# Kernel tuning notes

Measured on AMD Instinct MI355X. Metric: run time of the kernel, lower is better.

Reference implementation:

```python
import jax, jax.numpy as jnp
import numpy as np

DIM = 1024
H = 8            # heads (light and heavy)
DH = 64          # dim_head
W = 64           # local attention window (light_window_size // 2)
NQ = 512         # num_heavy_tokens_q
NKV = 1024       # num_heavy_tokens_kv
EPS = 1.0        # coor descent eps
NITERS = 50      # coor descent iters
FETCH = 9.0 / 8.0
SCALE = DH ** -0.5


def _ln(x, w, b):
    m = x.mean(-1, keepdims=True)
    v = ((x - m) ** 2).mean(-1, keepdims=True)
    return (x - m) * jax.lax.rsqrt(v + 1e-5) * w + b


def _rms(x, g):
    n = jnp.maximum(jnp.linalg.norm(x, axis=-1, keepdims=True), 1e-12)
    return x / n * np.sqrt(DIM).astype(np.float32) * g


def local_attn(x, Wqkv, Wout):
    # LocalMHA, non-causal, look_backward=1, look_forward=1, window W
    b, n, _ = x.shape
    nw = n // W
    qkv = x @ Wqkv.T                      # [b,n,3*H*DH]
    q, k, v = jnp.split(qkv, 3, axis=-1)
    def towin(t):
        return t.reshape(b, nw, W, H, DH).transpose(0, 3, 1, 2, 4)  # [b,h,nw,w,dh]
    q, k, v = map(towin, (q, k, v))
    def expand(t):  # gather prev/cur/next windows -> [b,h,nw,3w,dh]
        tp = jnp.pad(t, ((0, 0), (0, 0), (1, 1), (0, 0), (0, 0)))
        return jnp.concatenate([tp[:, :, :-2], tp[:, :, 1:-1], tp[:, :, 2:]], axis=3)
    ke, ve = expand(k), expand(v)
    sim = jnp.einsum('bhnid,bhnjd->bhnij', q, ke) * SCALE
    win = jnp.arange(nw)
    valid = jnp.concatenate([
        jnp.repeat((win > 0)[:, None], W, 1),
        jnp.ones((nw, W), bool),
        jnp.repeat((win < nw - 1)[:, None], W, 1)], axis=1)  # [nw,3w]
    sim = jnp.where(valid[None, None, :, None, :], sim, -1e9)
    attn = jax.nn.softmax(sim, axis=-1)
    o = jnp.einsum('bhnij,bhnjd->bhnid', attn, ve)
    o = o.transpose(0, 2, 3, 1, 4).reshape(b, n, H * DH)
    return o @ Wout.T


def route(x, routing_token, num_tokens):
    # CoordinateDescentRouter with num_routing_tokens=1, straight_through=True
    s = jnp.einsum('bnd,rd->brn', x, routing_token).reshape(x.shape[0], x.shape[1])
    n = s.shape[-1]
    logk = jnp.log(jnp.asarray(min(num_tokens * FETCH, float(n)), s.dtype))
    def body(ab, _):
        a, bb = ab
        a = EPS * (logk - jax.nn.logsumexp((s + bb) / EPS, axis=-1, keepdims=True))
        bb = -jax.nn.relu(s + a)
        return (a, bb), None
    (a, bb), _ = jax.lax.scan(body, (jnp.zeros((s.shape[0], 1), s.dtype), -s), None, length=NITERS)
    scores = jnp.exp((s + a + bb) / EPS)
    sel_scores, sel_idx = jax.lax.top_k(scores, num_tokens)
    # straight-through: forward value 1.0, gradient of identity
    sel_scores = sel_scores + jax.lax.stop_gradient(1.0 - sel_scores)
    return sel_scores, sel_idx


def heavy_attn(xq, ctx, scores_kv, gamma, Wq, Wkv, Wout, null_kv):
    b = xq.shape[0]
    xq = _rms(xq, gamma)
    ctx = _rms(ctx, gamma)
    q = (xq @ Wq.T).reshape(b, -1, H, DH).transpose(0, 2, 1, 3)           # [b,h,nq,dh]
    kv = (ctx @ Wkv.T).reshape(b, -1, H, 2 * DH).transpose(0, 2, 1, 3)    # [b,h,nkv,2dh]
    k, v = kv[..., :DH], kv[..., DH:]
    v = v * scores_kv[:, None, :, None]
    nk = jnp.broadcast_to(null_kv[0][None, :, None, :], (b, H, 1, DH))
    nv = jnp.broadcast_to(null_kv[1][None, :, None, :], (b, H, 1, DH))
    k = jnp.concatenate([nk, k], axis=2)
    v = jnp.concatenate([nv, v], axis=2)
    sim = jnp.einsum('bhid,bhjd->bhij', q, k) * SCALE
    attn = jax.nn.softmax(sim, axis=-1)
    o = jnp.einsum('bhij,bhjd->bhid', attn, v)
    o = o.transpose(0, 2, 1, 3).reshape(b, -1, H * DH)
    return o @ Wout.T


def setup_inputs() -> dict:
    key = jax.random.key(0)
    ks = jax.random.split(key, 12)
    D, IN = DIM, H * DH
    w = lambda k, shape: jax.random.normal(k, shape, jnp.float32) * 0.02
    return {
        'x': jax.random.normal(ks[0], (4, 4096, D), jnp.float32),
        'ln_w': jnp.ones((D,), jnp.float32),
        'ln_b': jnp.zeros((D,), jnp.float32),
        'Wqkv': w(ks[1], (3 * IN, D)),
        'Wout_l': w(ks[2], (D, IN)),
        'rt_q': jax.random.normal(ks[3], (1, D), jnp.float32),
        'rt_kv': jax.random.normal(ks[4], (1, D), jnp.float32),
        'gamma': jnp.ones((D,), jnp.float32),
        'Wq': w(ks[5], (IN, D)),
        'Wkv': w(ks[6], (2 * IN, D)),
        'Wout_h': w(ks[7], (D, IN)),
        'null_kv': jax.random.normal(ks[8], (2, H, DH), jnp.float32),
        'null_q': jax.random.normal(ks[9], (D,), jnp.float32),
    }


def reference(x, ln_w, ln_b, Wqkv, Wout_l, rt_q, rt_kv, gamma, Wq, Wkv, Wout_h, null_kv, null_q):
    b, n, d = x.shape
    light = local_attn(_ln(x, ln_w, ln_b), Wqkv, Wout_l)
    sq, iq = route(x, rt_q, NQ)
    skv, ikv = route(x, rt_kv, NKV)
    br = jnp.arange(b)[:, None]
    xq = x[br, iq]          # gather routed queries  [b,NQ,d]
    xkv = x[br, ikv]        # gather routed kv       [b,NKV,d]
    heavy = heavy_attn(xq, xkv, skv, gamma, Wq, Wkv, Wout_h, null_kv)
    heavy = heavy * sq[..., None]
    out = jnp.broadcast_to(null_q[None, None, :], (b, n, d))
    out = out.at[br, iq].set(heavy)   # scatter heavy branch back
    return out + light
```

## Files before the change

kernel.cpp:

```cpp
#include <hip/hip_runtime.h>
#include <hip/hip_bf16.h>

typedef __attribute__((ext_vector_type(8))) short bv8;
typedef __attribute__((ext_vector_type(4))) float fv4;
typedef __hip_bfloat16 bf16;

#define MFMA16(a,b,c) __builtin_amdgcn_mfma_f32_16x16x32_bf16((a),(b),(c),0,0,0)
#define GLOAD_LDS(gp, lp) __builtin_amdgcn_global_load_lds( \
    (const __attribute__((address_space(1))) void*)(gp), \
    (__attribute__((address_space(3))) void*)(lp), 16, 0, 0)

template<int NW>
__device__ __forceinline__ float blockReduceSumF(float v) {
  #pragma unroll
  for (int m = 1; m < 64; m <<= 1) v += __shfl_xor(v, m, 64);
  __shared__ float sm[NW];
  if ((threadIdx.x & 63) == 0) sm[threadIdx.x >> 6] = v;
  __syncthreads();
  float t = 0.f;
  #pragma unroll
  for (int i = 0; i < NW; ++i) t += sm[i];
  __syncthreads();
  return t;
}

template<int NW>
__device__ __forceinline__ double blockReduceMaxD(double v) {
  #pragma unroll
  for (int m = 1; m < 64; m <<= 1) v = fmax(v, __shfl_xor(v, m, 64));
  __shared__ double sm[NW];
  if ((threadIdx.x & 63) == 0) sm[threadIdx.x >> 6] = v;
  __syncthreads();
  double t = sm[0];
  #pragma unroll
  for (int i = 1; i < NW; ++i) t = fmax(t, sm[i]);
  __syncthreads();
  return t;
}

__global__ __launch_bounds__(256)
void prep_kernel(const float* __restrict__ x, const float* __restrict__ lnw,
                 const float* __restrict__ lnb, const float* __restrict__ rtq,
                 const float* __restrict__ rtkv, bf16* __restrict__ lnout,
                 double* __restrict__ s,
                 const float* __restrict__ a0, const float* __restrict__ a1,
                 const float* __restrict__ a2, const float* __restrict__ a3,
                 const float* __restrict__ a4,
                 bf16* __restrict__ b0, bf16* __restrict__ b1, bf16* __restrict__ b2,
                 bf16* __restrict__ b3, bf16* __restrict__ b4,
                 int* __restrict__ posq) {
  const int bid = blockIdx.x;
  if (bid < 16384) {
    const int r = bid;
    const float* xr = x + (size_t)r * 1024;
    float v4[4]; float ssum = 0.f;
    double dq = 0.0, dk = 0.0;
    #pragma unroll
    for (int i = 0; i < 4; ++i) {
      int d = threadIdx.x + i * 256;
      float v = xr[d];
      v4[i] = v; ssum += v;
      dq += (double)v * (double)rtq[d];
      dk += (double)v * (double)rtkv[d];
    }
    ssum = blockReduceSumF<4>(ssum);
    const float mean = ssum * (1.0f / 1024.0f);
    float vs = 0.f;
    #pragma unroll
    for (int i = 0; i < 4; ++i) { float d = v4[i] - mean; vs += d * d; }
    vs = blockReduceSumF<4>(vs);
    const float rstd = 1.0f / sqrtf(vs * (1.0f / 1024.0f) + 1e-5f);
    #pragma unroll
    for (int m = 1; m < 64; m <<= 1) { dq += __shfl_xor(dq, m, 64); dk += __shfl_xor(dk, m, 64); }
    __shared__ double smq[4], smk[4];
    if ((threadIdx.x & 63) == 0) { smq[threadIdx.x >> 6] = dq; smk[threadIdx.x >> 6] = dk; }
    __syncthreads();
    if (threadIdx.x == 0) {
      s[r] = smq[0] + smq[1] + smq[2] + smq[3];
      s[16384 + r] = smk[0] + smk[1] + smk[2] + smk[3];
    }
    bf16* orow = lnout + (size_t)r * 1024;
    #pragma unroll
    for (int i = 0; i < 4; ++i) {
      int d = threadIdx.x + i * 256;
      orow[d] = __float2bfloat16((v4[i] - mean) * rstd * lnw[d] + lnb[d]);
    }
  } else if (bid < 18432) {
    size_t g = ((size_t)(bid - 16384) * 256 + threadIdx.x) * 8;
    const float* src; bf16* dst; size_t off;
    if (g < 1572864)      { src = a0; dst = b0; off = g; }
    else if (g < 2097152) { src = a1; dst = b1; off = g - 1572864; }
    else if (g < 2621440) { src = a2; dst = b2; off = g - 2097152; }
    else if (g < 3670016) { src = a3; dst = b3; off = g - 2621440; }
    else                  { src = a4; dst = b4; off = g - 3670016; }
    float4 v0 = *(const float4*)(src + off);
    float4 v1 = *(const float4*)(src + off + 4);
    bv8 o;
    ((bf16*)&o)[0] = __float2bfloat16(v0.x); ((bf16*)&o)[1] = __float2bfloat16(v0.y);
    ((bf16*)&o)[2] = __float2bfloat16(v0.z); ((bf16*)&o)[3] = __float2bfloat16(v0.w);
    ((bf16*)&o)[4] = __float2bfloat16(v1.x); ((bf16*)&o)[5] = __float2bfloat16(v1.y);
    ((bf16*)&o)[6] = __float2bfloat16(v1.z); ((bf16*)&o)[7] = __float2bfloat16(v1.w);
    *(bv8*)(dst + off) = o;
  } else {
    int i0 = (bid - 18432) * 1024 + threadIdx.x * 4;
    posq[i0] = -1; posq[i0 + 1] = -1; posq[i0 + 2] = -1; posq[i0 + 3] = -1;
  }
}

__global__ __launch_bounds__(256, 1)
void route_sel_kernel(const double* __restrict__ s_all, int* __restrict__ iq,
                      int* __restrict__ ikv, int* __restrict__ posq) {
  const int route = blockIdx.x >> 2, b = blockIdx.x & 3;
  const double* s = s_all + route * 16384 + b * 4096;
  const double K = (route == 0) ? 576.0 : 1152.0;
  const int KSEL = (route == 0) ? 512 : 1024;
  const int tid = threadIdx.x;
  const int lane = tid & 63, wid = tid >> 6;
  __shared__ double evbuf[4096];
  __shared__ double a_sh;
  __shared__ int scn[256];

  double sv[16];
  #pragma unroll
  for (int i = 0; i < 16; ++i) sv[i] = s[tid * 16 + i];
  double mx = sv[0];
  #pragma unroll
  for (int i = 1; i < 16; ++i) mx = fmax(mx, sv[i]);
  mx = blockReduceMaxD<4>(mx);
  #pragma unroll
  for (int i = 0; i < 16; ++i) evbuf[tid * 16 + i] = exp(sv[i] - mx);
  __syncthreads();

  if (wid == 0) {
    double e64[64];
    #pragma unroll
    for (int j = 0; j < 64; ++j) e64[j] = evbuf[j * 64 + lane];
    double z = (4096.0 / K) * exp(-mx);
    for (int it = 1; it < 50; ++it) {
      double a0 = 0.0, a1 = 0.0, a2 = 0.0, a3 = 0.0;
      #pragma unroll
      for (int j = 0; j < 64; j += 4) {
        a0 += fmin(e64[j], z);
        a1 += fmin(e64[j + 1], z);
        a2 += fmin(e64[j + 2], z);
        a3 += fmin(e64[j + 3], z);
      }
      double t = (a0 + a1) + (a2 + a3);
      #pragma unroll
      for (int m = 1; m < 64; m <<= 1) t += __shfl_xor(t, m, 64);
      z = t / K;
    }
    if (lane == 0) a_sh = -mx - log(z);
  }
  __syncthreads();
  const double a = a_sh;

  float scf[16]; int m16 = 0;
  #pragma unroll
  for (int i = 0; i < 16; ++i) {
    scf[i] = (float)exp(fmin(sv[i] + a, 0.0));
    m16 += (scf[i] == 1.0f) ? 1 : 0;
  }
  scn[tid] = m16;
  __syncthreads();
  for (int off = 1; off < 256; off <<= 1) {
    int v = (tid >= off) ? scn[tid - off] : 0;
    __syncthreads();
    scn[tid] += v;
    __syncthreads();
  }
  const int total = scn[255];
  const int excl = scn[tid] - m16;
  if (total >= KSEL) {
    int rk = excl;
    #pragma unroll
    for (int i = 0; i < 16; ++i) {
      if (scf[i] == 1.0f) {
        if (rk < KSEL) {
          int idx = tid * 16 + i;
          if (route == 0) { iq[b * 512 + rk] = idx; posq[b * 4096 + idx] = rk; }
          else            { ikv[b * 1024 + rk] = idx; }
        }
        rk++;
      }
    }
  } else {
    unsigned long long* keys = (unsigned long long*)evbuf;
    #pragma unroll
    for (int i = 0; i < 16; ++i) {
      unsigned bits = __float_as_uint(scf[i]);
      keys[tid * 16 + i] = ((unsigned long long)(~bits) << 32) | (unsigned long long)(tid * 16 + i);
    }
    for (int k = 2; k <= 4096; k <<= 1) {
      for (int j = k >> 1; j > 0; j >>= 1) {
        __syncthreads();
        for (int t = tid; t < 2048; t += 256) {
          int i2 = ((t & ~(j - 1)) << 1) | (t & (j - 1));
          int ip = i2 + j;
          unsigned long long av = keys[i2], bvv = keys[ip];
          bool up = ((i2 & k) == 0);
          if (up ? (av > bvv) : (av < bvv)) { keys[i2] = bvv; keys[ip] = av; }
        }
      }
    }
    __syncthreads();
    for (int j2 = tid; j2 < KSEL; j2 += 256) {
      int idx = (int)(keys[j2] & 0xFFFFFFFFull);
      if (route == 0) { iq[b * 512 + j2] = idx; posq[b * 4096 + idx] = j2; }
      else            { ikv[b * 1024 + j2] = idx; }
    }
  }
}

template<int EPI>
__device__ __forceinline__ void gemm_core(
    const bf16* __restrict__ A, const bf16* __restrict__ B, void* __restrict__ Cout,
    int N, int K, int row0, int col0, bf16* As, bf16* Bs,
    const int* __restrict__ posq, const float* __restrict__ heavy,
    const float* __restrict__ nullq) {
  const int tid = threadIdx.x;
  const int lane = tid & 63, w = tid >> 6;
  const int wr = w >> 1, wc = w & 1;
  const int lrow = lane & 15, lk = (lane >> 4) * 8;
  fv4 acc[4][4];
  #pragma unroll
  for (int m = 0; m < 4; ++m)
    #pragma unroll
    for (int n = 0; n < 4; ++n) acc[m][n] = (fv4){0.f, 0.f, 0.f, 0.f};
  const int ob0 = w * 2048;
  for (int k0 = 0; k0 < K; k0 += 32) {
    #pragma unroll
    for (int t = 0; t < 2; ++t) {
      int ob = ob0 + t * 1024;
      int ofl = ob + lane * 16;
      int r = ofl >> 6, c8 = ((ofl >> 4) & 3) * 8;
      GLOAD_LDS(A + (size_t)(row0 + r) * K + k0 + c8, (char*)As + ob);
      GLOAD_LDS(B + (size_t)(col0 + r) * K + k0 + c8, (char*)Bs + ob);
    }
    __syncthreads();
    bv8 af[4], bfr[4];
    #pragma unroll
    for (int m = 0; m < 4; ++m) af[m] = *(bv8*)&As[(wr * 64 + m * 16 + lrow) * 32 + lk];
    #pragma unroll
    for (int n = 0; n < 4; ++n) bfr[n] = *(bv8*)&Bs[(wc * 64 + n * 16 + lrow) * 32 + lk];
    #pragma unroll
    for (int m = 0; m < 4; ++m)
      #pragma unroll
      for (int n = 0; n < 4; ++n)
        acc[m][n] = MFMA16(af[m], bfr[n], acc[m][n]);
    __syncthreads();
  }
  #pragma unroll
  for (int m = 0; m < 4; ++m) {
    int gr0 = row0 + wr * 64 + m * 16 + (lane >> 4) * 4;
    #pragma unroll
    for (int n = 0; n < 4; ++n) {
      int gc = col0 + wc * 64 + n * 16 + lrow;
      #pragma unroll
      for (int r = 0; r < 4; ++r) {
        int grow = gr0 + r;
        float vv = acc[m][n][r];
        if (EPI == 0) {
          ((bf16*)Cout)[(size_t)grow * N + gc] = __float2bfloat16(vv);
        } else if (EPI == 1) {
          ((float*)Cout)[(size_t)grow * N + gc] = vv;
        } else {
          int p = posq[grow];
          float add = (p >= 0) ? heavy[((size_t)((grow >> 12) * 512 + p)) * 1024 + gc]
                               : nullq[gc];
          ((float*)Cout)[(size_t)grow * N + gc] = vv + add;
        }
      }
    }
  }
}

__device__ __forceinline__ void xcd_remap(int d, int gx, int& row0, int& col0) {
  int q = d >> 3;
  col0 = (q % gx) * 128;
  row0 = ((d & 7) + 8 * (q / gx)) * 128;
}

template<int EPI>
__global__ __launch_bounds__(256)
void gemm_bt(const bf16* __restrict__ A, const bf16* __restrict__ B, void* __restrict__ Cout,
             int N, int K,
             const int* __restrict__ posq, const float* __restrict__ heavy,
             const float* __restrict__ nullq) {
  __shared__ alignas(16) bf16 As[128 * 32];
  __shared__ alignas(16) bf16 Bs[128 * 32];
  int row0, col0;
  xcd_remap(blockIdx.y * gridDim.x + blockIdx.x, gridDim.x, row0, col0);
  gemm_core<EPI>(A, B, Cout, N, K, row0, col0, As, Bs, posq, heavy, nullq);
}

__global__ __launch_bounds__(256)
void qkv_gather_kernel(const bf16* __restrict__ ln, const bf16* __restrict__ Wqkv,
                       bf16* __restrict__ qkv,
                       const float* __restrict__ x, const float* __restrict__ gamma,
                       const int* __restrict__ iq, const int* __restrict__ ikv,
                       bf16* __restrict__ xq, bf16* __restrict__ xkv) {
  const int bid = blockIdx.x;
  const int tid = threadIdx.x;
  if (bid < 1536) {
    __shared__ alignas(16) bf16 As[128 * 32];
    __shared__ alignas(16) bf16 Bs[128 * 32];
    int row0, col0;
    xcd_remap(bid, 12, row0, col0);
    gemm_core<0>(ln, Wqkv, qkv, 1536, 1024, row0, col0, As, Bs, nullptr, nullptr, nullptr);
  } else {
    const int gid = bid - 1536;
    const float* src; bf16* dst;
    if (gid < 2048) {
      int b = gid >> 9, j = gid & 511;
      int tok = iq[b * 512 + j];
      src = x + ((size_t)(b * 4096 + tok)) * 1024;
      dst = xq + (size_t)gid * 1024;
    } else {
      int id = gid - 2048;
      int b = id >> 10, j = id & 1023;
      int tok = ikv[b * 1024 + j];
      src = x + ((size_t)(b * 4096 + tok)) * 1024;
      dst = xkv + (size_t)id * 1024;
    }
    float v4[4]; float ss = 0.f;
    #pragma unroll
    for (int i = 0; i < 4; ++i) { v4[i] = src[tid + i * 256]; ss += v4[i] * v4[i]; }
    ss = blockReduceSumF<4>(ss);
    const float nrm = fmaxf(sqrtf(ss), 1e-12f);
    const float scl = 32.0f / nrm;
    #pragma unroll
    for (int i = 0; i < 4; ++i) {
      int d = tid + i * 256;
      dst[d] = __float2bfloat16(v4[i] * scl * gamma[d]);
    }
  }
}

__global__ __launch_bounds__(256)
void la_wqkv_kernel(const bf16* __restrict__ qkv, bf16* __restrict__ olight,
                    const bf16* __restrict__ xkv, const bf16* __restrict__ Wkv,
                    bf16* __restrict__ kvh,
                    const bf16* __restrict__ xq, const bf16* __restrict__ Wq,
                    bf16* __restrict__ qh) {
  __shared__ __align__(16) char smem_raw[36864];
  const int tid = threadIdx.x;
  const int bid = blockIdx.x;
  if (bid < 320) {
    bf16* As = (bf16*)smem_raw;
    bf16* Bs = (bf16*)(smem_raw + 8192);
    int row0, col0;
    if (bid < 256) {
      xcd_remap(bid, 8, row0, col0);
      gemm_core<0>(xkv, Wkv, kvh, 1024, 1024, row0, col0, As, Bs, nullptr, nullptr, nullptr);
    } else {
      xcd_remap(bid - 256, 4, row0, col0);
      gemm_core<0>(xq, Wq, qh, 512, 1024, row0, col0, As, Bs, nullptr, nullptr, nullptr);
    }
  } else {
    const int lid = bid - 320;
    const int w = lid & 63, h = (lid >> 6) & 7, b = lid >> 9;
    const int lane = tid & 63, wv = tid >> 6;
    const int lrow = lane & 15, lkg = lane >> 4;
    typedef bf16 row72[72];
    row72* Qs  = (row72*)smem_raw;
    row72* Ks  = (row72*)(smem_raw + 9216);
    row72* Vts = (row72*)(smem_raw + 18432);
    row72* Ps  = (row72*)(smem_raw + 27648);
    {
      const size_t baseq = ((size_t)(b * 4096 + w * 64)) * 1536 + h * 64;
      #pragma unroll
      for (int v = 0; v < 2; ++v) {
        int vec = tid + v * 256; int i = vec >> 3, dd = (vec & 7) * 8;
        *(bv8*)&Qs[i][dd] = *(const bv8*)&qkv[baseq + (size_t)i * 1536 + dd];
      }
    }
    fv4 oacc[4];
    float m_run[4], l_run[4];
    #pragma unroll
    for (int n = 0; n < 4; ++n) oacc[n] = (fv4){0.f, 0.f, 0.f, 0.f};
    #pragma unroll
    for (int r = 0; r < 4; ++r) { m_run[r] = -INFINITY; l_run[r] = 0.f; }
    for (int c = 0; c < 3; ++c) {
      int sw = w - 1 + c;
      if (sw < 0 || sw >= 64) continue;
      __syncthreads();
      const size_t bkv = ((size_t)(b * 4096 + sw * 64)) * 1536 + h * 64;
      #pragma unroll
      for (int v = 0; v < 2; ++v) {
        int vec = tid + v * 256; int i = vec >> 3, dd = (vec & 7) * 8;
        *(bv8*)&Ks[i][dd] = *(const bv8*)&qkv[bkv + 512 + (size_t)i * 1536 + dd];
      }
      #pragma unroll
      for (int v = 0; v < 2; ++v) {
        int vec = tid + v * 256; int j = vec >> 3, d0 = (vec & 7) * 8;
        bv8 val = *(const bv8*)&qkv[bkv + 1024 + (size_t)j * 1536 + d0];
        #pragma unroll
        for (int i = 0; i < 8; ++i) Vts[d0 + i][j] = ((bf16*)&val)[i];
      }
      __syncthreads();
      fv4 sa[4];
      #pragma unroll
      for (int n = 0; n < 4; ++n) {
        sa[n] = (fv4){0.f, 0.f, 0.f, 0.f};
        #pragma unroll
        for (int ks = 0; ks < 2; ++ks) {
          bv8 aq = *(bv8*)&Qs[wv * 16 + lrow][lkg * 8 + ks * 32];
          bv8 bk = *(bv8*)&Ks[n * 16 + lrow][lkg * 8 + ks * 32];
          sa[n] = MFMA16(aq, bk, sa[n]);
        }
      }
      float mc[4];
      #pragma unroll
      for (int r = 0; r < 4; ++r) {
        #pragma unroll
        for (int n = 0; n < 4; ++n) sa[n][r] *= 0.125f;
        mc[r] = fmaxf(fmaxf(sa[0][r], sa[1][r]), fmaxf(sa[2][r], sa[3][r]));
      }
      #pragma unroll
      for (int m = 1; m < 16; m <<= 1)
        #pragma unroll
        for (int r = 0; r < 4; ++r) mc[r] = fmaxf(mc[r], __shfl_xor(mc[r], m, 64));
      float p[4][4], ls[4];
      #pragma unroll
      for (int r = 0; r < 4; ++r) {
        float mn = fmaxf(m_run[r], mc[r]);
        float scl = expf(m_run[r] - mn);
        ls[r] = 0.f;
        #pragma unroll
        for (int n = 0; n < 4; ++n) { p[n][r] = expf(sa[n][r] - mn); ls[r] += p[n][r]; }
        m_run[r] = mn;
        l_run[r] *= scl;
        #pragma unroll
        for (int n = 0; n < 4; ++n) oacc[n][r] *= scl;
      }
      #pragma unroll
      for (int m = 1; m < 16; m <<= 1)
        #pragma unroll
        for (int r = 0; r < 4; ++r) ls[r] += __shfl_xor(ls[r], m, 64);
      #pragma unroll
      for (int r = 0; r < 4; ++r) l_run[r] += ls[r];
      #pragma unroll
      for (int n = 0; n < 4; ++n)
        #pragma unroll
        for (int r = 0; r < 4; ++r)
          Ps[wv * 16 + lkg * 4 + r][n * 16 + lrow] = __float2bfloat16(p[n][r]);
      __syncthreads();
      #pragma unroll
      for (int n = 0; n < 4; ++n)
        #pragma unroll
        for (int ks = 0; ks < 2; ++ks) {
          bv8 ap = *(bv8*)&Ps[wv * 16 + lrow][lkg * 8 + ks * 32];
          bv8 bvv = *(bv8*)&Vts[n * 16 + lrow][lkg * 8 + ks * 32];
          oacc[n] = MFMA16(ap, bvv, oacc[n]);
        }
    }
    const size_t ob = ((size_t)(b * 4096 + w * 64 + wv * 16)) * 512 + h * 64;
    #pragma unroll
    for (int n = 0; n < 4; ++n)
      #pragma unroll
      for (int r = 0; r < 4; ++r) {
        int row = lkg * 4 + r;
        olight[ob + (size_t)row * 512 + n * 16 + lrow] = __float2bfloat16(oacc[n][r] / l_run[r]);
      }
  }
}

__global__ __launch_bounds__(256)
void heavy_attn_split_kernel(const bf16* __restrict__ qh, const bf16* __restrict__ kvh,
                             const float* __restrict__ nkv, bf16* __restrict__ o_part,
                             float* __restrict__ ml_part) {
  const int qt = blockIdx.x, h = blockIdx.y;
  const int b = blockIdx.z >> 2, s = blockIdx.z & 3;
  const int tid = threadIdx.x;
  const int lane = tid & 63, wv = tid >> 6;
  const int lrow = lane & 15, lkg = lane >> 4;
  __shared__ bf16 Qs[64][72], Ks[64][72], Vts[64][72], Ps[64][72];
  {
    const size_t baseq = ((size_t)(b * 512 + qt * 64)) * 512 + h * 64;
    #pragma unroll
    for (int v = 0; v < 2; ++v) {
      int vec = tid + v * 256; int i = vec >> 3, dd = (vec & 7) * 8;
      *(bv8*)&Qs[i][dd] = *(const bv8*)&qh[baseq + (size_t)i * 512 + dd];
    }
  }
  fv4 oacc[4];
  float m_run[4], l_run[4];
  #pragma unroll
  for (int n = 0; n < 4; ++n) oacc[n] = (fv4){0.f, 0.f, 0.f, 0.f};
  #pragma unroll
  for (int r = 0; r < 4; ++r) { m_run[r] = -INFINITY; l_run[r] = 0.f; }
  const int cs = (s == 0) ? 0 : (s * 4 + 1);
  const int ce = s * 4 + 5;
  for (int c = cs; c < ce; ++c) {
    __syncthreads();
    #pragma unroll
    for (int v = 0; v < 2; ++v) {
      int vec = tid + v * 256; int j = vec >> 3, dd = (vec & 7) * 8;
      int kvg = c * 64 + j;
      bv8 val;
      if (kvg >= 1 && kvg <= 1024) {
        val = *(const bv8*)&kvh[((size_t)(b * 1024 + kvg - 1)) * 1024 + h * 128 + dd];
      } else if (kvg == 0) {
        #pragma unroll
        for (int t = 0; t < 8; ++t) ((bf16*)&val)[t] = __float2bfloat16(nkv[h * 64 + dd + t]);
      } else {
        #pragma unroll
        for (int t = 0; t < 8; ++t) ((short*)&val)[t] = 0;
      }
      *(bv8*)&Ks[j][dd] = val;
    }
    #pragma unroll
    for (int v = 0; v < 2; ++v) {
      int vec = tid + v * 256; int j = vec >> 3, d0 = (vec & 7) * 8;
      int kvg = c * 64 + j;
      if (kvg >= 1 && kvg <= 1024) {
        bv8 val = *(const bv8*)&kvh[((size_t)(b * 1024 + kvg - 1)) * 1024 + h * 128 + 64 + d0];
        #pragma unroll
        for (int i = 0; i < 8; ++i) Vts[d0 + i][j] = ((bf16*)&val)[i];
      } else if (kvg == 0) {
        #pragma unroll
        for (int i = 0; i < 8; ++i) Vts[d0 + i][j] = __float2bfloat16(nkv[512 + h * 64 + d0 + i]);
      } else {
        #pragma unroll
        for (int i = 0; i < 8; ++i) Vts[d0 + i][j] = __float2bfloat16(0.0f);
      }
    }
    __syncthreads();
    fv4 sa[4];
    #pragma unroll
    for (int n = 0; n < 4; ++n) {
      sa[n] = (fv4){0.f, 0.f, 0.f, 0.f};
      #pragma unroll
      for (int ks = 0; ks < 2; ++ks) {
        bv8 aq = *(bv8*)&Qs[wv * 16 + lrow][lkg * 8 + ks * 32];
        bv8 bk = *(bv8*)&Ks[n * 16 + lrow][lkg * 8 + ks * 32];
        sa[n] = MFMA16(aq, bk, sa[n]);
      }
    }
    float mc[4];
    #pragma unroll
    for (int r = 0; r < 4; ++r) {
      #pragma unroll
      for (int n = 0; n < 4; ++n) {
        sa[n][r] *= 0.125f;
        int kvg = c * 64 + n * 16 + lrow;
        if (kvg > 1024) sa[n][r] = -1e30f;
      }
      mc[r] = fmaxf(fmaxf(sa[0][r], sa[1][r]), fmaxf(sa[2][r], sa[3][r]));
    }
    #pragma unroll
    for (int m = 1; m < 16; m <<= 1)
      #pragma unroll
      for (int r = 0; r < 4; ++r) mc[r] = fmaxf(mc[r], __shfl_xor(mc[r], m, 64));
    float p[4][4], ls[4];
    #pragma unroll
    for (int r = 0; r < 4; ++r) {
      float mn = fmaxf(m_run[r], mc[r]);
      float scl = expf(m_run[r] - mn);
      ls[r] = 0.f;
      #pragma unroll
      for (int n = 0; n < 4; ++n) { p[n][r] = expf(sa[n][r] - mn); ls[r] += p[n][r]; }
      m_run[r] = mn;
      l_run[r] *= scl;
      #pragma unroll
      for (int n = 0; n < 4; ++n) oacc[n][r] *= scl;
    }
    #pragma unroll
    for (int m = 1; m < 16; m <<= 1)
      #pragma unroll
      for (int r = 0; r < 4; ++r) ls[r] += __shfl_xor(ls[r], m, 64);
    #pragma unroll
    for (int r = 0; r < 4; ++r) l_run[r] += ls[r];
    #pragma unroll
    for (int n = 0; n < 4; ++n)
      #pragma unroll
      for (int r = 0; r < 4; ++r)
        Ps[wv * 16 + lkg * 4 + r][n * 16 + lrow] = __float2bfloat16(p[n][r]);
    __syncthreads();
    #pragma unroll
    for (int n = 0; n < 4; ++n)
      #pragma unroll
      for (int ks = 0; ks < 2; ++ks) {
        bv8 ap = *(bv8*)&Ps[wv * 16 + lrow][lkg * 8 + ks * 32];
        bv8 bvv = *(bv8*)&Vts[n * 16 + lrow][lkg * 8 + ks * 32];
        oacc[n] = MFMA16(ap, bvv, oacc[n]);
      }
  }
  const int idx = (((s * 4 + b) * 8 + h) * 8 + qt);
  bf16* ob = o_part + (size_t)idx * 4096;
  #pragma unroll
  for (int n = 0; n < 4; ++n)
    #pragma unroll
    for (int r = 0; r < 4; ++r) {
      int row = wv * 16 + lkg * 4 + r;
      ob[row * 64 + n * 16 + lrow] = __float2bfloat16(oacc[n][r]);
    }
  if (lrow == 0) {
    #pragma unroll
    for (int r = 0; r < 4; ++r) {
      int row = wv * 16 + lkg * 4 + r;
      ml_part[idx * 128 + row] = m_run[r];
      ml_part[idx * 128 + 64 + row] = l_run[r];
    }
  }
}

__global__ __launch_bounds__(256)
void wouth_gemm_kernel(const bf16* __restrict__ o_part, const float* __restrict__ ml_part,
                       const bf16* __restrict__ B, float* __restrict__ Cout) {
  __shared__ alignas(16) bf16 As[128 * 32];
  __shared__ alignas(16) bf16 Bs[128 * 32];
  const int N = 1024, K = 512;
  int row0, col0;
  xcd_remap(blockIdx.y * gridDim.x + blockIdx.x, gridDim.x, row0, col0);
  const int tid = threadIdx.x;
  const int lane = tid & 63, w = tid >> 6;
  const int wr = w >> 1, wc = w & 1;
  const int lrow = lane & 15, lk = (lane >> 4) * 8;
  fv4 acc[4][4];
  #pragma unroll
  for (int m = 0; m < 4; ++m)
    #pragma unroll
    for (int n = 0; n < 4; ++n) acc[m][n] = (fv4){0.f, 0.f, 0.f, 0.f};
  const int ob0 = w * 2048;
  for (int k0 = 0; k0 < K; k0 += 32) {
    #pragma unroll
    for (int t = 0; t < 2; ++t) {
      int ob = ob0 + t * 1024;
      int ofl = ob + lane * 16;
      int r = ofl >> 6, c8 = ((ofl >> 4) & 3) * 8;
      int grow = row0 + r, k = k0 + c8;
      int b = grow >> 9, qrow = grow & 511;
      int qt = qrow >> 6, row_in = qrow & 63;
      int h = k >> 6, d0 = k & 63;
      bv8 v[4]; float m[4], l[4];
      #pragma unroll
      for (int s = 0; s < 4; ++s) {
        int idx = (((s * 4 + b) * 8 + h) * 8 + qt);
        v[s] = *(const bv8*)&o_part[(size_t)idx * 4096 + row_in * 64 + d0];
        m[s] = ml_part[idx * 128 + row_in];
        l[s] = ml_part[idx * 128 + 64 + row_in];
      }
      float mstar = fmaxf(fmaxf(m[0], m[1]), fmaxf(m[2], m[3]));
      float ws[4]; float wsum = 0.f;
      #pragma unroll
      for (int s = 0; s < 4; ++s) { ws[s] = expf(m[s] - mstar); wsum += ws[s] * l[s]; }
      const float inv = 1.0f / wsum;
      bv8 o8;
      #pragma unroll
      for (int j = 0; j < 8; ++j) {
        float acc8 = 0.f;
        #pragma unroll
        for (int s = 0; s < 4; ++s) acc8 += ws[s] * __bfloat162float(((bf16*)&v[s])[j]);
        ((bf16*)&o8)[j] = __float2bfloat16(acc8 * inv);
      }
      *(bv8*)((char*)As + ofl) = o8;
      GLOAD_LDS(B + (size_t)(col0 + r) * K + k0 + c8, (char*)Bs + ob);
    }
    __syncthreads();
    bv8 af[4], bfr[4];
    #pragma unroll
    for (int m2 = 0; m2 < 4; ++m2) af[m2] = *(bv8*)&As[(wr * 64 + m2 * 16 + lrow) * 32 + lk];
    #pragma unroll
    for (int n = 0; n < 4; ++n) bfr[n] = *(bv8*)&Bs[(wc * 64 + n * 16 + lrow) * 32 + lk];
    #pragma unroll
    for (int m2 = 0; m2 < 4; ++m2)
      #pragma unroll
      for (int n = 0; n < 4; ++n)
        acc[m2][n] = MFMA16(af[m2], bfr[n], acc[m2][n]);
    __syncthreads();
  }
  #pragma unroll
  for (int m2 = 0; m2 < 4; ++m2) {
    int gr0 = row0 + wr * 64 + m2 * 16 + (lane >> 4) * 4;
    #pragma unroll
    for (int n = 0; n < 4; ++n) {
      int gc = col0 + wc * 64 + n * 16 + lrow;
      #pragma unroll
      for (int r = 0; r < 4; ++r)
        Cout[(size_t)(gr0 + r) * N + gc] = acc[m2][n][r];
    }
  }
}

extern "C" void kernel_launch(void* const* d_in, const int* in_sizes, int n_in,
                              void* d_out, int out_size, void* d_ws, size_t ws_size,
                              hipStream_t stream) {
  (void)in_sizes; (void)n_in; (void)out_size; (void)ws_size;
  const float* x     = (const float*)d_in[0];
  const float* ln_w  = (const float*)d_in[1];
  const float* ln_b  = (const float*)d_in[2];
  const float* Wqkv  = (const float*)d_in[3];
  const float* Woutl = (const float*)d_in[4];
  const float* rtq   = (const float*)d_in[5];
  const float* rtkv  = (const float*)d_in[6];
  const float* gamma = (const float*)d_in[7];
  const float* Wq    = (const float*)d_in[8];
  const float* Wkv   = (const float*)d_in[9];
  const float* Wouth = (const float*)d_in[10];
  const float* nkv   = (const float*)d_in[11];
  const float* nq    = (const float*)d_in[12];
  float* out = (float*)d_out;

  char* ws = (char*)d_ws;
  size_t off = 0;
  auto alloc = [&](size_t bytes) -> void* {
    void* p = ws + off;
    off = (off + bytes + 255) & ~(size_t)255;
    return p;
  };
  bf16* ln_bf    = (bf16*)alloc(16384ull * 1024 * 2);
  bf16* qkv_bf   = (bf16*)alloc(16384ull * 1536 * 2);
  bf16* ol_bf    = (bf16*)alloc(16384ull * 512 * 2);
  bf16* Wqkv_bf  = (bf16*)alloc(1536ull * 1024 * 2);
  bf16* Woutl_bf = (bf16*)alloc(1024ull * 512 * 2);
  bf16* Wq_bf    = (bf16*)alloc(512ull * 1024 * 2);
  bf16* Wkv_bf   = (bf16*)alloc(1024ull * 1024 * 2);
  bf16* Wouth_bf = (bf16*)alloc(1024ull * 512 * 2);
  double* s_d    = (double*)alloc(32768ull * 8);
  int* iq        = (int*)alloc(2048ull * 4);
  int* ikv       = (int*)alloc(4096ull * 4);
  int* posq      = (int*)alloc(16384ull * 4);
  bf16* xq_bf    = (bf16*)alloc(2048ull * 1024 * 2);
  bf16* xkv_bf   = (bf16*)alloc(4096ull * 1024 * 2);
  bf16* qh_bf    = (bf16*)alloc(2048ull * 512 * 2);
  bf16* kvh_bf   = (bf16*)alloc(4096ull * 1024 * 2);
  float* heavy_f = (float*)alloc(2048ull * 1024 * 4);
  bf16* o_part   = (bf16*)alloc(4096ull * 4096 * 2);
  float* ml_part = (float*)alloc(4096ull * 128 * 4);

  prep_kernel<<<18448, 256, 0, stream>>>(x, ln_w, ln_b, rtq, rtkv, ln_bf, s_d,
                                         Wqkv, Woutl, Wq, Wkv, Wouth,
                                         Wqkv_bf, Woutl_bf, Wq_bf, Wkv_bf, Wouth_bf,
                                         posq);

  route_sel_kernel<<<8, 256, 0, stream>>>(s_d, iq, ikv, posq);

  qkv_gather_kernel<<<7680, 256, 0, stream>>>(ln_bf, Wqkv_bf, qkv_bf,
                                              x, gamma, iq, ikv, xq_bf, xkv_bf);

  la_wqkv_kernel<<<2368, 256, 0, stream>>>(qkv_bf, ol_bf,
                                           xkv_bf, Wkv_bf, kvh_bf,
                                           xq_bf, Wq_bf, qh_bf);

  heavy_attn_split_kernel<<<dim3(8, 8, 16), 256, 0, stream>>>(qh_bf, kvh_bf, nkv, o_part, ml_part);

  wouth_gemm_kernel<<<dim3(8, 16), 256, 0, stream>>>(o_part, ml_part, Wouth_bf, heavy_f);

  gemm_bt<2><<<dim3(8, 128), 256, 0, stream>>>(ol_bf, Woutl_bf, out, 1024, 512,
                                               posq, heavy_f, nq);
}
```

Measured before the change: 287.1 us.

## Fuse routing into QKV GEMM launch, regroup gather with local attention, widen GEMM K tile

The routing-selection kernel now runs as 8 extra blocks inside the QKV GEMM launch, so routing overlaps with the GEMM instead of taking a serial single-wave launch. Its coordinate-descent loop is spread over all 256 threads using a shared-memory reduction. The row gather/convert now shares a launch with local attention, and the heavy Wq/Wkv GEMMs get their own launch. The shared GEMM core moves from a 32-wide to a 64-wide K tile with an XOR-swizzled LDS layout, halving the number of barrier rounds and reducing bank conflicts, at the cost of twice the LDS per block.

```diff
diff --git a/kernel.cpp b/kernel.cpp
--- a/kernel.cpp
+++ b/kernel.cpp
@@ -107,111 +107,6 @@
   }
 }
 
-__global__ __launch_bounds__(256, 1)
-void route_sel_kernel(const double* __restrict__ s_all, int* __restrict__ iq,
-                      int* __restrict__ ikv, int* __restrict__ posq) {
-  const int route = blockIdx.x >> 2, b = blockIdx.x & 3;
-  const double* s = s_all + route * 16384 + b * 4096;
-  const double K = (route == 0) ? 576.0 : 1152.0;
-  const int KSEL = (route == 0) ? 512 : 1024;
-  const int tid = threadIdx.x;
-  const int lane = tid & 63, wid = tid >> 6;
-  __shared__ double evbuf[4096];
-  __shared__ double a_sh;
-  __shared__ int scn[256];
-
-  double sv[16];
-  #pragma unroll
-  for (int i = 0; i < 16; ++i) sv[i] = s[tid * 16 + i];
-  double mx = sv[0];
-  #pragma unroll
-  for (int i = 1; i < 16; ++i) mx = fmax(mx, sv[i]);
-  mx = blockReduceMaxD<4>(mx);
-  #pragma unroll
-  for (int i = 0; i < 16; ++i) evbuf[tid * 16 + i] = exp(sv[i] - mx);
-  __syncthreads();
-
-  if (wid == 0) {
-    double e64[64];
-    #pragma unroll
-    for (int j = 0; j < 64; ++j) e64[j] = evbuf[j * 64 + lane];
-    double z = (4096.0 / K) * exp(-mx);
-    for (int it = 1; it < 50; ++it) {
-      double a0 = 0.0, a1 = 0.0, a2 = 0.0, a3 = 0.0;
-      #pragma unroll
-      for (int j = 0; j < 64; j += 4) {
-        a0 += fmin(e64[j], z);
-        a1 += fmin(e64[j + 1], z);
-        a2 += fmin(e64[j + 2], z);
-        a3 += fmin(e64[j + 3], z);
-      }
-      double t = (a0 + a1) + (a2 + a3);
-      #pragma unroll
-      for (int m = 1; m < 64; m <<= 1) t += __shfl_xor(t, m, 64);
-      z = t / K;
-    }
-    if (lane == 0) a_sh = -mx - log(z);
-  }
-  __syncthreads();
-  const double a = a_sh;
-
-  float scf[16]; int m16 = 0;
-  #pragma unroll
-  for (int i = 0; i < 16; ++i) {
-    scf[i] = (float)exp(fmin(sv[i] + a, 0.0));
-    m16 += (scf[i] == 1.0f) ? 1 : 0;
-  }
-  scn[tid] = m16;
-  __syncthreads();
-  for (int off = 1; off < 256; off <<= 1) {
-    int v = (tid >= off) ? scn[tid - off] : 0;
-    __syncthreads();
-    scn[tid] += v;
-    __syncthreads();
-  }
-  const int total = scn[255];
-  const int excl = scn[tid] - m16;
-  if (total >= KSEL) {
-    int rk = excl;
-    #pragma unroll
-    for (int i = 0; i < 16; ++i) {
-      if (scf[i] == 1.0f) {
-        if (rk < KSEL) {
-          int idx = tid * 16 + i;
-          if (route == 0) { iq[b * 512 + rk] = idx; posq[b * 4096 + idx] = rk; }
-          else            { ikv[b * 1024 + rk] = idx; }
-        }
-        rk++;
-      }
-    }
-  } else {
-    unsigned long long* keys = (unsigned long long*)evbuf;
-    #pragma unroll
-    for (int i = 0; i < 16; ++i) {
-      unsigned bits = __float_as_uint(scf[i]);
-      keys[tid * 16 + i] = ((unsigned long long)(~bits) << 32) | (unsigned long long)(tid * 16 + i);
-    }
-    for (int k = 2; k <= 4096; k <<= 1) {
-      for (int j = k >> 1; j > 0; j >>= 1) {
-        __syncthreads();
-        for (int t = tid; t < 2048; t += 256) {
-          int i2 = ((t & ~(j - 1)) << 1) | (t & (j - 1));
-          int ip = i2 + j;
-          unsigned long long av = keys[i2], bvv = keys[ip];
-          bool up = ((i2 & k) == 0);
-          if (up ? (av > bvv) : (av < bvv)) { keys[i2] = bvv; keys[ip] = av; }
-        }
-      }
-    }
-    __syncthreads();
-    for (int j2 = tid; j2 < KSEL; j2 += 256) {
-      int idx = (int)(keys[j2] & 0xFFFFFFFFull);
-      if (route == 0) { iq[b * 512 + j2] = idx; posq[b * 4096 + idx] = j2; }
-      else            { ikv[b * 1024 + j2] = idx; }
-    }
-  }
-}
-
 template<int EPI>
 __device__ __forceinline__ void gemm_core(
     const bf16* __restrict__ A, const bf16* __restrict__ B, void* __restrict__ Cout,
@@ -221,33 +116,43 @@
   const int tid = threadIdx.x;
   const int lane = tid & 63, w = tid >> 6;
   const int wr = w >> 1, wc = w & 1;
-  const int lrow = lane & 15, lk = (lane >> 4) * 8;
+  const int lrow = lane & 15, lkg = lane >> 4;
   fv4 acc[4][4];
   #pragma unroll
   for (int m = 0; m < 4; ++m)
     #pragma unroll
     for (int n = 0; n < 4; ++n) acc[m][n] = (fv4){0.f, 0.f, 0.f, 0.f};
-  const int ob0 = w * 2048;
-  for (int k0 = 0; k0 < K; k0 += 32) {
-    #pragma unroll
-    for (int t = 0; t < 2; ++t) {
-      int ob = ob0 + t * 1024;
-      int ofl = ob + lane * 16;
-      int r = ofl >> 6, c8 = ((ofl >> 4) & 3) * 8;
-      GLOAD_LDS(A + (size_t)(row0 + r) * K + k0 + c8, (char*)As + ob);
-      GLOAD_LDS(B + (size_t)(col0 + r) * K + k0 + c8, (char*)Bs + ob);
-    }
-    __syncthreads();
-    bv8 af[4], bfr[4];
-    #pragma unroll
-    for (int m = 0; m < 4; ++m) af[m] = *(bv8*)&As[(wr * 64 + m * 16 + lrow) * 32 + lk];
-    #pragma unroll
-    for (int n = 0; n < 4; ++n) bfr[n] = *(bv8*)&Bs[(wc * 64 + n * 16 + lrow) * 32 + lk];
-    #pragma unroll
-    for (int m = 0; m < 4; ++m)
-      #pragma unroll
-      for (int n = 0; n < 4; ++n)
-        acc[m][n] = MFMA16(af[m], bfr[n], acc[m][n]);
+  const int ob0 = w * 1024;
+  for (int k0 = 0; k0 < K; k0 += 64) {
+    #pragma unroll
+    for (int t = 0; t < 4; ++t) {
+      int ob = t * 4096 + ob0;
+      int byteL = ob + lane * 16;
+      int r = byteL >> 7;
+      int cU = ((byteL >> 4) & 7) ^ (r & 7);
+      GLOAD_LDS(A + (size_t)(row0 + r) * K + k0 + cU * 8, (char*)As + ob);
+      GLOAD_LDS(B + (size_t)(col0 + r) * K + k0 + cU * 8, (char*)Bs + ob);
+    }
+    __syncthreads();
+    #pragma unroll
+    for (int ks = 0; ks < 2; ++ks) {
+      bv8 af[4], bfr[4];
+      #pragma unroll
+      for (int m = 0; m < 4; ++m) {
+        int row = wr * 64 + m * 16 + lrow;
+        af[m] = *(bv8*)((char*)As + row * 128 + (((ks * 4 + lkg) ^ (row & 7)) << 4));
+      }
+      #pragma unroll
+      for (int n = 0; n < 4; ++n) {
+        int row = wc * 64 + n * 16 + lrow;
+        bfr[n] = *(bv8*)((char*)Bs + row * 128 + (((ks * 4 + lkg) ^ (row & 7)) << 4));
+      }
+      #pragma unroll
+      for (int m = 0; m < 4; ++m)
+        #pragma unroll
+        for (int n = 0; n < 4; ++n)
+          acc[m][n] = MFMA16(af[m], bfr[n], acc[m][n]);
+    }
     __syncthreads();
   }
   #pragma unroll
@@ -287,29 +192,226 @@
              int N, int K,
              const int* __restrict__ posq, const float* __restrict__ heavy,
              const float* __restrict__ nullq) {
-  __shared__ alignas(16) bf16 As[128 * 32];
-  __shared__ alignas(16) bf16 Bs[128 * 32];
+  __shared__ alignas(16) bf16 As[128 * 64];
+  __shared__ alignas(16) bf16 Bs[128 * 64];
   int row0, col0;
   xcd_remap(blockIdx.y * gridDim.x + blockIdx.x, gridDim.x, row0, col0);
   gemm_core<EPI>(A, B, Cout, N, K, row0, col0, As, Bs, posq, heavy, nullq);
 }
 
 __global__ __launch_bounds__(256)
-void qkv_gather_kernel(const bf16* __restrict__ ln, const bf16* __restrict__ Wqkv,
-                       bf16* __restrict__ qkv,
-                       const float* __restrict__ x, const float* __restrict__ gamma,
-                       const int* __restrict__ iq, const int* __restrict__ ikv,
-                       bf16* __restrict__ xq, bf16* __restrict__ xkv) {
+void qkv_route_kernel(const bf16* __restrict__ ln, const bf16* __restrict__ Wqkv,
+                      bf16* __restrict__ qkv,
+                      const double* __restrict__ s_all, int* __restrict__ iq,
+                      int* __restrict__ ikv, int* __restrict__ posq) {
+  __shared__ __align__(16) char arena[34816];
   const int bid = blockIdx.x;
   const int tid = threadIdx.x;
-  if (bid < 1536) {
-    __shared__ alignas(16) bf16 As[128 * 32];
-    __shared__ alignas(16) bf16 Bs[128 * 32];
+  if (bid >= 8) {
+    bf16* As = (bf16*)arena;
+    bf16* Bs = (bf16*)(arena + 16384);
     int row0, col0;
-    xcd_remap(bid, 12, row0, col0);
+    xcd_remap(bid - 8, 12, row0, col0);
     gemm_core<0>(ln, Wqkv, qkv, 1536, 1024, row0, col0, As, Bs, nullptr, nullptr, nullptr);
   } else {
-    const int gid = bid - 1536;
+    const int route = bid >> 2, b = bid & 3;
+    const double* s = s_all + route * 16384 + b * 4096;
+    const double Kk = (route == 0) ? 576.0 : 1152.0;
+    const int KSEL = (route == 0) ? 512 : 1024;
+    const int lane = tid & 63, wid = tid >> 6;
+    unsigned long long* keys = (unsigned long long*)arena;
+    int* scn = (int*)(arena + 32768);
+    double* red = (double*)(arena + 33792);
+    double sv[16];
+    #pragma unroll
+    for (int i = 0; i < 16; ++i) sv[i] = s[tid * 16 + i];
+    double mx = sv[0];
+    #pragma unroll
+    for (int i = 1; i < 16; ++i) mx = fmax(mx, sv[i]);
+    mx = blockReduceMaxD<4>(mx);
+    double ev[16];
+    #pragma unroll
+    for (int i = 0; i < 16; ++i) ev[i] = exp(sv[i] - mx);
+    double z = (4096.0 / Kk) * exp(-mx);
+    for (int it = 1; it < 50; ++it) {
+      double t0 = 0.0, t1 = 0.0;
+      #pragma unroll
+      for (int i = 0; i < 16; i += 2) { t0 += fmin(ev[i], z); t1 += fmin(ev[i + 1], z); }
+      double t = t0 + t1;
+      #pragma unroll
+      for (int m = 1; m < 64; m <<= 1) t += __shfl_xor(t, m, 64);
+      if (lane == 0) red[wid] = t;
+      __syncthreads();
+      z = (red[0] + red[1] + red[2] + red[3]) / Kk;
+      __syncthreads();
+    }
+    const double a = -mx - log(z);
+    float scf[16]; int m16 = 0;
+    #pragma unroll
+    for (int i = 0; i < 16; ++i) {
+      scf[i] = (float)exp(fmin(sv[i] + a, 0.0));
+      m16 += (scf[i] == 1.0f) ? 1 : 0;
+    }
+    scn[tid] = m16;
+    __syncthreads();
+    for (int off = 1; off < 256; off <<= 1) {
+      int v = (tid >= off) ? scn[tid - off] : 0;
+      __syncthreads();
+      scn[tid] += v;
+      __syncthreads();
+    }
+    const int total = scn[255];
+    const int excl = scn[tid] - m16;
+    if (total >= KSEL) {
+      int rk = excl;
+      #pragma unroll
+      for (int i = 0; i < 16; ++i) {
+        if (scf[i] == 1.0f) {
+          if (rk < KSEL) {
+            int idx = tid * 16 + i;
+            if (route == 0) { iq[b * 512 + rk] = idx; posq[b * 4096 + idx] = rk; }
+            else            { ikv[b * 1024 + rk] = idx; }
+          }
+          rk++;
+        }
+      }
+    } else {
+      #pragma unroll
+      for (int i = 0; i < 16; ++i) {
+        unsigned bits = __float_as_uint(scf[i]);
+        keys[tid * 16 + i] = ((unsigned long long)(~bits) << 32) | (unsigned long long)(tid * 16 + i);
+      }
+      for (int k = 2; k <= 4096; k <<= 1) {
+        for (int j = k >> 1; j > 0; j >>= 1) {
+          __syncthreads();
+          for (int t = tid; t < 2048; t += 256) {
+            int i2 = ((t & ~(j - 1)) << 1) | (t & (j - 1));
+            int ip = i2 + j;
+            unsigned long long av = keys[i2], bvv = keys[ip];
+            bool up = ((i2 & k) == 0);
+            if (up ? (av > bvv) : (av < bvv)) { keys[i2] = bvv; keys[ip] = av; }
+          }
+        }
+      }
+      __syncthreads();
+      for (int j2 = tid; j2 < KSEL; j2 += 256) {
+        int idx = (int)(keys[j2] & 0xFFFFFFFFull);
+        if (route == 0) { iq[b * 512 + j2] = idx; posq[b * 4096 + idx] = j2; }
+        else            { ikv[b * 1024 + j2] = idx; }
+      }
+    }
+  }
+}
+
+__global__ __launch_bounds__(256)
+void la_gather_kernel(const bf16* __restrict__ qkv, bf16* __restrict__ olight,
+                      const float* __restrict__ x, const float* __restrict__ gamma,
+                      const int* __restrict__ iq, const int* __restrict__ ikv,
+                      bf16* __restrict__ xq, bf16* __restrict__ xkv) {
+  __shared__ bf16 Qs[64][72], Ks[64][72], Vts[64][72], Ps[64][72];
+  const int tid = threadIdx.x;
+  if (blockIdx.x < 2048) {
+    const int w = blockIdx.x & 63, h = (blockIdx.x >> 6) & 7, b = blockIdx.x >> 9;
+    const int lane = tid & 63, wv = tid >> 6;
+    const int lrow = lane & 15, lkg = lane >> 4;
+    {
+      const size_t baseq = ((size_t)(b * 4096 + w * 64)) * 1536 + h * 64;
+      #pragma unroll
+      for (int v = 0; v < 2; ++v) {
+        int vec = tid + v * 256; int i = vec >> 3, dd = (vec & 7) * 8;
+        *(bv8*)&Qs[i][dd] = *(const bv8*)&qkv[baseq + (size_t)i * 1536 + dd];
+      }
+    }
+    fv4 oacc[4];
+    float m_run[4], l_run[4];
+    #pragma unroll
+    for (int n = 0; n < 4; ++n) oacc[n] = (fv4){0.f, 0.f, 0.f, 0.f};
+    #pragma unroll
+    for (int r = 0; r < 4; ++r) { m_run[r] = -INFINITY; l_run[r] = 0.f; }
+    for (int c = 0; c < 3; ++c) {
+      int sw = w - 1 + c;
+      if (sw < 0 || sw >= 64) continue;
+      __syncthreads();
+      const size_t bkv = ((size_t)(b * 4096 + sw * 64)) * 1536 + h * 64;
+      #pragma unroll
+      for (int v = 0; v < 2; ++v) {
+        int vec = tid + v * 256; int i = vec >> 3, dd = (vec & 7) * 8;
+        *(bv8*)&Ks[i][dd] = *(const bv8*)&qkv[bkv + 512 + (size_t)i * 1536 + dd];
+      }
+      #pragma unroll
+      for (int v = 0; v < 2; ++v) {
+        int vec = tid + v * 256; int j = vec >> 3, d0 = (vec & 7) * 8;
+        bv8 val = *(const bv8*)&qkv[bkv + 1024 + (size_t)j * 1536 + d0];
+        #pragma unroll
+        for (int i = 0; i < 8; ++i) Vts[d0 + i][j] = ((bf16*)&val)[i];
+      }
+      __syncthreads();
+      fv4 sa[4];
+      #pragma unroll
+      for (int n = 0; n < 4; ++n) {
+        sa[n] = (fv4){0.f, 0.f, 0.f, 0.f};
+        #pragma unroll
+        for (int ks = 0; ks < 2; ++ks) {
+          bv8 aq = *(bv8*)&Qs[wv * 16 + lrow][lkg * 8 + ks * 32];
+          bv8 bk = *(bv8*)&Ks[n * 16 + lrow][lkg * 8 + ks * 32];
+          sa[n] = MFMA16(aq, bk, sa[n]);
+        }
+      }
+      float mc[4];
+      #pragma unroll
+      for (int r = 0; r < 4; ++r) {
+        #pragma unroll
+        for (int n = 0; n < 4; ++n) sa[n][r] *= 0.125f;
+        mc[r] = fmaxf(fmaxf(sa[0][r], sa[1][r]), fmaxf(sa[2][r], sa[3][r]));
+      }
+      #pragma unroll
+      for (int m = 1; m < 16; m <<= 1)
+        #pragma unroll
+        for (int r = 0; r < 4; ++r) mc[r] = fmaxf(mc[r], __shfl_xor(mc[r], m, 64));
+      float p[4][4], ls[4];
+      #pragma unroll
+      for (int r = 0; r < 4; ++r) {
+        float mn = fmaxf(m_run[r], mc[r]);
+        float scl = expf(m_run[r] - mn);
+        ls[r] = 0.f;
+        #pragma unroll
+        for (int n = 0; n < 4; ++n) { p[n][r] = expf(sa[n][r] - mn); ls[r] += p[n][r]; }
+        m_run[r] = mn;
+        l_run[r] *= scl;
+        #pragma unroll
+        for (int n = 0; n < 4; ++n) oacc[n][r] *= scl;
+      }
+      #pragma unroll
+      for (int m = 1; m < 16; m <<= 1)
+        #pragma unroll
+        for (int r = 0; r < 4; ++r) ls[r] += __shfl_xor(ls[r], m, 64);
+      #pragma unroll
+      for (int r = 0; r < 4; ++r) l_run[r] += ls[r];
+      #pragma unroll
+      for (int n = 0; n < 4; ++n)
+        #pragma unroll
+        for (int r = 0; r < 4; ++r)
+          Ps[wv * 16 + lkg * 4 + r][n * 16 + lrow] = __float2bfloat16(p[n][r]);
+      __syncthreads();
+      #pragma unroll
+      for (int n = 0; n < 4; ++n)
+        #pragma unroll
+        for (int ks = 0; ks < 2; ++ks) {
+          bv8 ap = *(bv8*)&Ps[wv * 16 + lrow][lkg * 8 + ks * 32];
+          bv8 bvv = *(bv8*)&Vts[n * 16 + lrow][lkg * 8 + ks * 32];
+          oacc[n] = MFMA16(ap, bvv, oacc[n]);
+        }
+    }
+    const size_t ob = ((size_t)(b * 4096 + w * 64 + wv * 16)) * 512 + h * 64;
+    #pragma unroll
+    for (int n = 0; n < 4; ++n)
+      #pragma unroll
+      for (int r = 0; r < 4; ++r) {
+        int row = lkg * 4 + r;
+        olight[ob + (size_t)row * 512 + n * 16 + lrow] = __float2bfloat16(oacc[n][r] / l_run[r]);
+      }
+  } else {
+    const int gid = blockIdx.x - 2048;
     const float* src; bf16* dst;
     if (gid < 2048) {
       int b = gid >> 9, j = gid & 511;
@@ -338,131 +440,20 @@
 }
 
 __global__ __launch_bounds__(256)
-void la_wqkv_kernel(const bf16* __restrict__ qkv, bf16* __restrict__ olight,
-                    const bf16* __restrict__ xkv, const bf16* __restrict__ Wkv,
-                    bf16* __restrict__ kvh,
-                    const bf16* __restrict__ xq, const bf16* __restrict__ Wq,
-                    bf16* __restrict__ qh) {
-  __shared__ __align__(16) char smem_raw[36864];
-  const int tid = threadIdx.x;
+void wqkv_kernel(const bf16* __restrict__ xkv, const bf16* __restrict__ Wkv,
+                 bf16* __restrict__ kvh,
+                 const bf16* __restrict__ xq, const bf16* __restrict__ Wq,
+                 bf16* __restrict__ qh) {
+  __shared__ alignas(16) bf16 As[128 * 64];
+  __shared__ alignas(16) bf16 Bs[128 * 64];
   const int bid = blockIdx.x;
-  if (bid < 320) {
-    bf16* As = (bf16*)smem_raw;
-    bf16* Bs = (bf16*)(smem_raw + 8192);
-    int row0, col0;
-    if (bid < 256) {
-      xcd_remap(bid, 8, row0, col0);
-      gemm_core<0>(xkv, Wkv, kvh, 1024, 1024, row0, col0, As, Bs, nullptr, nullptr, nullptr);
-    } else {
-      xcd_remap(bid - 256, 4, row0, col0);
-      gemm_core<0>(xq, Wq, qh, 512, 1024, row0, col0, As, Bs, nullptr, nullptr, nullptr);
-    }
+  int row0, col0;
+  if (bid < 256) {
+    xcd_remap(bid, 8, row0, col0);
+    gemm_core<0>(xkv, Wkv, kvh, 1024, 1024, row0, col0, As, Bs, nullptr, nullptr, nullptr);
   } else {
-    const int lid = bid - 320;
-    const int w = lid & 63, h = (lid >> 6) & 7, b = lid >> 9;
-    const int lane = tid & 63, wv = tid >> 6;
-    const int lrow = lane & 15, lkg = lane >> 4;
-    typedef bf16 row72[72];
-    row72* Qs  = (row72*)smem_raw;
-    row72* Ks  = (row72*)(smem_raw + 9216);
-    row72* Vts = (row72*)(smem_raw + 18432);
-    row72* Ps  = (row72*)(smem_raw + 27648);
-    {
-      const size_t baseq = ((size_t)(b * 4096 + w * 64)) * 1536 + h * 64;
-      #pragma unroll
-      for (int v = 0; v < 2; ++v) {
-        int vec = tid + v * 256; int i = vec >> 3, dd = (vec & 7) * 8;
-        *(bv8*)&Qs[i][dd] = *(const bv8*)&qkv[baseq + (size_t)i * 1536 + dd];
-      }
-    }
-    fv4 oacc[4];
-    float m_run[4], l_run[4];
-    #pragma unroll
-    for (int n = 0; n < 4; ++n) oacc[n] = (fv4){0.f, 0.f, 0.f, 0.f};
-    #pragma unroll
-    for (int r = 0; r < 4; ++r) { m_run[r] = -INFINITY; l_run[r] = 0.f; }
-    for (int c = 0; c < 3; ++c) {
-      int sw = w - 1 + c;
-      if (sw < 0 || sw >= 64) continue;
-      __syncthreads();
-      const size_t bkv = ((size_t)(b * 4096 + sw * 64)) * 1536 + h * 64;
-      #pragma unroll
-      for (int v = 0; v < 2; ++v) {
-        int vec = tid + v * 256; int i = vec >> 3, dd = (vec & 7) * 8;
-        *(bv8*)&Ks[i][dd] = *(const bv8*)&qkv[bkv + 512 + (size_t)i * 1536 + dd];
-      }
-      #pragma unroll
-      for (int v = 0; v < 2; ++v) {
-        int vec = tid + v * 256; int j = vec >> 3, d0 = (vec & 7) * 8;
-        bv8 val = *(const bv8*)&qkv[bkv + 1024 + (size_t)j * 1536 + d0];
-        #pragma unroll
-        for (int i = 0; i < 8; ++i) Vts[d0 + i][j] = ((bf16*)&val)[i];
-      }
-      __syncthreads();
-      fv4 sa[4];
-      #pragma unroll
-      for (int n = 0; n < 4; ++n) {
-        sa[n] = (fv4){0.f, 0.f, 0.f, 0.f};
-        #pragma unroll
-        for (int ks = 0; ks < 2; ++ks) {
-          bv8 aq = *(bv8*)&Qs[wv * 16 + lrow][lkg * 8 + ks * 32];
-          bv8 bk = *(bv8*)&Ks[n * 16 + lrow][lkg * 8 + ks * 32];
-          sa[n] = MFMA16(aq, bk, sa[n]);
-        }
-      }
-      float mc[4];
-      #pragma unroll
-      for (int r = 0; r < 4; ++r) {
-        #pragma unroll
-        for (int n = 0; n < 4; ++n) sa[n][r] *= 0.125f;
-        mc[r] = fmaxf(fmaxf(sa[0][r], sa[1][r]), fmaxf(sa[2][r], sa[3][r]));
-      }
-      #pragma unroll
-      for (int m = 1; m < 16; m <<= 1)
-        #pragma unroll
-        for (int r = 0; r < 4; ++r) mc[r] = fmaxf(mc[r], __shfl_xor(mc[r], m, 64));
-      float p[4][4], ls[4];
-      #pragma unroll
-      for (int r = 0; r < 4; ++r) {
-        float mn = fmaxf(m_run[r], mc[r]);
-        float scl = expf(m_run[r] - mn);
-        ls[r] = 0.f;
-        #pragma unroll
-        for (int n = 0; n < 4; ++n) { p[n][r] = expf(sa[n][r] - mn); ls[r] += p[n][r]; }
-        m_run[r] = mn;
-        l_run[r] *= scl;
-        #pragma unroll
-        for (int n = 0; n < 4; ++n) oacc[n][r] *= scl;
-      }
-      #pragma unroll
-      for (int m = 1; m < 16; m <<= 1)
-        #pragma unroll
-        for (int r = 0; r < 4; ++r) ls[r] += __shfl_xor(ls[r], m, 64);
-      #pragma unroll
-      for (int r = 0; r < 4; ++r) l_run[r] += ls[r];
-      #pragma unroll
-      for (int n = 0; n < 4; ++n)
-        #pragma unroll
-        for (int r = 0; r < 4; ++r)
-          Ps[wv * 16 + lkg * 4 + r][n * 16 + lrow] = __float2bfloat16(p[n][r]);
-      __syncthreads();
-      #pragma unroll
-      for (int n = 0; n < 4; ++n)
-        #pragma unroll
-        for (int ks = 0; ks < 2; ++ks) {
-          bv8 ap = *(bv8*)&Ps[wv * 16 + lrow][lkg * 8 + ks * 32];
-          bv8 bvv = *(bv8*)&Vts[n * 16 + lrow][lkg * 8 + ks * 32];
-          oacc[n] = MFMA16(ap, bvv, oacc[n]);
-        }
-    }
-    const size_t ob = ((size_t)(b * 4096 + w * 64 + wv * 16)) * 512 + h * 64;
-    #pragma unroll
-    for (int n = 0; n < 4; ++n)
-      #pragma unroll
-      for (int r = 0; r < 4; ++r) {
-        int row = lkg * 4 + r;
-        olight[ob + (size_t)row * 512 + n * 16 + lrow] = __float2bfloat16(oacc[n][r] / l_run[r]);
-      }
+    xcd_remap(bid - 256, 4, row0, col0);
+    gemm_core<0>(xq, Wq, qh, 512, 1024, row0, col0, As, Bs, nullptr, nullptr, nullptr);
   }
 }
 
@@ -735,14 +726,12 @@
                                          Wqkv_bf, Woutl_bf, Wq_bf, Wkv_bf, Wouth_bf,
                                          posq);
 
-  route_sel_kernel<<<8, 256, 0, stream>>>(s_d, iq, ikv, posq);
-
-  qkv_gather_kernel<<<7680, 256, 0, stream>>>(ln_bf, Wqkv_bf, qkv_bf,
-                                              x, gamma, iq, ikv, xq_bf, xkv_bf);
-
-  la_wqkv_kernel<<<2368, 256, 0, stream>>>(qkv_bf, ol_bf,
-                                           xkv_bf, Wkv_bf, kvh_bf,
-                                           xq_bf, Wq_bf, qh_bf);
+  qkv_route_kernel<<<1544, 256, 0, stream>>>(ln_bf, Wqkv_bf, qkv_bf,
+                                             s_d, iq, ikv, posq);
+
+  la_gather_kernel<<<8192, 256, 0, stream>>>(qkv_bf, ol_bf, x, gamma, iq, ikv, xq_bf, xkv_bf);
+
+  wqkv_kernel<<<320, 256, 0, stream>>>(xkv_bf, Wkv_bf, kvh_bf, xq_bf, Wq_bf, qh_bf);
 
   heavy_attn_split_kernel<<<dim3(8, 8, 16), 256, 0, stream>>>(qh_bf, kvh_bf, nkv, o_part, ml_part);
 
```

After: 273.1 us, median of 3. 4.9% less time.
